# Kernel optimization log

Hardware: AMD Instinct MI355X
Metric: run time of the kernel (lower is better)

Reference implementation:

```python
import jax, jax.numpy as jnp
import numpy as np

B, S, D, H, DFF = 2, 2048, 768, 12, 3072
HD = D // H
LN_EPS = 1e-5


def _layernorm(x, g, b):
    mu = jnp.mean(x, axis=-1, keepdims=True)
    var = jnp.mean((x - mu) ** 2, axis=-1, keepdims=True)
    return (x - mu) * jax.lax.rsqrt(var + LN_EPS) * g + b


def setup_inputs() -> dict:
    key = jax.random.key(0)
    ks = jax.random.split(key, 16)
    s_d = 1.0 / np.sqrt(D)
    s_ff = 1.0 / np.sqrt(DFF)
    return {
        "x": jax.random.normal(ks[0], (B, S, D), jnp.float32),
        "alibi_bias": jax.random.normal(ks[1], (H, S, S), jnp.float32) * 0.1,
        "Wq": jax.random.normal(ks[2], (D, D), jnp.float32) * s_d,
        "bq": jnp.zeros((D,), jnp.float32),
        "Wk": jax.random.normal(ks[3], (D, D), jnp.float32) * s_d,
        "bk": jnp.zeros((D,), jnp.float32),
        "Wv": jax.random.normal(ks[4], (D, D), jnp.float32) * s_d,
        "bv": jnp.zeros((D,), jnp.float32),
        "Wo": jax.random.normal(ks[5], (D, D), jnp.float32) * s_d,
        "bo": jnp.zeros((D,), jnp.float32),
        "W1": jax.random.normal(ks[6], (D, DFF), jnp.float32) * s_d,
        "b1": jnp.zeros((DFF,), jnp.float32),
        "W2": jax.random.normal(ks[7], (DFF, D), jnp.float32) * s_ff,
        "b2": jnp.zeros((D,), jnp.float32),
        "g1": jnp.ones((D,), jnp.float32),
        "be1": jnp.zeros((D,), jnp.float32),
        "g2": jnp.ones((D,), jnp.float32),
        "be2": jnp.zeros((D,), jnp.float32),
    }


def reference(x, alibi_bias, Wq, bq, Wk, bk, Wv, bv, Wo, bo, W1, b1, W2, b2, g1, be1, g2, be2):
    # QKV projections -> (B, H, S, HD)
    def split_heads(t):
        return t.reshape(B, S, H, HD).transpose(0, 2, 1, 3)

    q = split_heads(x @ Wq + bq)
    k = split_heads(x @ Wk + bk)
    v = split_heads(x @ Wv + bv)

    # causal mask (S, S): -inf above diagonal
    causal = jnp.where(jnp.triu(jnp.ones((S, S), bool), k=1), -jnp.inf, 0.0).astype(x.dtype)
    mask = alibi_bias[None] + causal[None, None]  # (1, H, S, S) broadcast over batch

    scale = 1.0 / np.sqrt(HD)
    scores = jnp.einsum("bhqd,bhkd->bhqk", q, k) * scale + mask
    probs = jax.nn.softmax(scores, axis=-1)
    attn = jnp.einsum("bhqk,bhkd->bhqd", probs, v)  # (B, H, S, HD)
    attn = attn.transpose(0, 2, 1, 3).reshape(B, S, D)
    attn = attn @ Wo + bo

    x = _layernorm(x + attn, g1, be1)
    ff = jax.nn.relu(x @ W1 + b1) @ W2 + b2
    x = _layernorm(x + ff, g2, be2)
    return x
```

## Files before the change

kernel.cpp:

```cpp
#include <hip/hip_runtime.h>
#include <hip/hip_bf16.h>

#define BB 2
#define SS 2048
#define DD 768
#define HH 12
#define HD 64
#define DFF 3072
#define NROW (BB * SS)
#define QLD  2304
#define LN_EPS 1e-5f
#define NSPLIT 4

typedef __attribute__((ext_vector_type(8))) short bf16x8;
typedef __attribute__((ext_vector_type(4))) short bf16x4;
typedef __attribute__((ext_vector_type(4))) float f32x4;

__device__ __forceinline__ void gll16(const void* g, void* l) {
    __builtin_amdgcn_global_load_lds(
        (const __attribute__((address_space(1))) unsigned int*)g,
        (__attribute__((address_space(3))) unsigned int*)l,
        16, 0, 0);
}

__device__ __forceinline__ unsigned short bf16bits(float f) {
    __hip_bfloat16 h = __float2bfloat16(f);
    return *(unsigned short*)&h;
}

__device__ __forceinline__ float bf16tof(unsigned short u) {
    unsigned int ui = ((unsigned int)u) << 16;
    return __uint_as_float(ui);
}

__device__ __forceinline__ float block_sum(float v, float* red) {
    __syncthreads();
    #pragma unroll
    for (int off = 32; off > 0; off >>= 1) v += __shfl_down(v, off, 64);
    if ((threadIdx.x & 63) == 0) red[threadIdx.x >> 6] = v;
    __syncthreads();
    if (threadIdx.x == 0) red[0] = red[0] + red[1] + red[2] + red[3];
    __syncthreads();
    return red[0];
}

template<int TM, int TN>
__global__ __launch_bounds__(256) void mfma_gemm(
        const __hip_bfloat16* __restrict__ A, const __hip_bfloat16* __restrict__ BT,
        const float* __restrict__ bias, float* __restrict__ Cf,
        __hip_bfloat16* __restrict__ Cb,
        int N, int K, int relu, int bf16out, int qscale_cols) {
    constexpr int BK = 64;
    constexpr int MW = TM / 32;
    constexpr int NW = TN / 32;
    __shared__ __hip_bfloat16 a_s[TM * BK];
    __shared__ __hip_bfloat16 b_s[TN * BK];

    const int tid  = threadIdx.x;
    const int lane = tid & 63;
    const int wid  = tid >> 6;
    const int wm   = (wid & 1) * (TM / 2);
    const int wn   = (wid >> 1) * (TN / 2);
    const int qq   = lane & 15;
    const int quad = lane >> 4;

    const int nwg  = (int)(gridDim.x * gridDim.y);
    const int dlin = (int)blockIdx.x + (int)gridDim.x * (int)blockIdx.y;
    const int wsw  = (dlin & 7) * (nwg >> 3) + (dlin >> 3);
    const int m0 = (wsw / (int)gridDim.x) * TM;
    const int n0 = (wsw % (int)gridDim.x) * TN;

    const int r8   = lane >> 3;
    const int u8   = lane & 7;
    const int gcol = ((u8 ^ r8) << 3);

    f32x4 acc[MW][NW] = {};

    for (int k0 = 0; k0 < K; k0 += BK) {
        const __hip_bfloat16* Ag = A + (size_t)m0 * K + k0 + gcol;
        #pragma unroll
        for (int i = 0; i < TM / 32; i++) {
            const int row = i * 32 + wid * 8 + r8;
            gll16(Ag + (size_t)row * K, a_s + row * BK + u8 * 8);
        }
        const __hip_bfloat16* Bg = BT + (size_t)n0 * K + k0 + gcol;
        #pragma unroll
        for (int i = 0; i < TN / 32; i++) {
            const int row = i * 32 + wid * 8 + r8;
            gll16(Bg + (size_t)row * K, b_s + row * BK + u8 * 8);
        }
        __syncthreads();

        #pragma unroll
        for (int kh = 0; kh < 2; kh++) {
            const int ku = kh * 4 + quad;
            bf16x8 af[MW], bfr[NW];
            #pragma unroll
            for (int mi = 0; mi < MW; mi++) {
                const int row = wm + mi * 16 + qq;
                af[mi] = *(const bf16x8*)(a_s + row * BK + ((ku ^ (qq & 7)) << 3));
            }
            #pragma unroll
            for (int ni = 0; ni < NW; ni++) {
                const int row = wn + ni * 16 + qq;
                bfr[ni] = *(const bf16x8*)(b_s + row * BK + ((ku ^ (qq & 7)) << 3));
            }
            #pragma unroll
            for (int mi = 0; mi < MW; mi++)
                #pragma unroll
                for (int ni = 0; ni < NW; ni++)
                    acc[mi][ni] = __builtin_amdgcn_mfma_f32_16x16x32_bf16(
                            af[mi], bfr[ni], acc[mi][ni], 0, 0, 0);
        }
        __syncthreads();
    }

    #pragma unroll
    for (int mi = 0; mi < MW; mi++) {
        #pragma unroll
        for (int ni = 0; ni < NW; ni++) {
            const int col = n0 + wn + ni * 16 + qq;
            const float bv = bias[col];
            const float sc = (col < qscale_cols) ? 0.125f : 1.0f;
            #pragma unroll
            for (int r = 0; r < 4; r++) {
                const int row = m0 + wm + mi * 16 + quad * 4 + r;
                float v = acc[mi][ni][r] + bv;
                if (relu) v = fmaxf(v, 0.f);
                v *= sc;
                if (bf16out) Cb[(size_t)row * N + col] = __float2bfloat16(v);
                else         Cf[(size_t)row * N + col] = v;
            }
        }
    }
}

__device__ __forceinline__ void transpose_tile(
        const float* __restrict__ in, __hip_bfloat16* __restrict__ out,
        int K, int N, int tix, int tiy, float (*t)[33]) {
    const int n0 = tix * 32;
    const int k0 = tiy * 32;
    const int r = threadIdx.x >> 3;
    const int c = threadIdx.x & 7;
    float4 v = *(const float4*)&in[(size_t)(k0 + r) * N + n0 + c * 4];
    t[r][c * 4 + 0] = v.x;
    t[r][c * 4 + 1] = v.y;
    t[r][c * 4 + 2] = v.z;
    t[r][c * 4 + 3] = v.w;
    __syncthreads();
    union { unsigned short u[4]; uint2 w; } pk;
    #pragma unroll
    for (int j = 0; j < 4; j++) pk.u[j] = bf16bits(t[c * 4 + j][r]);
    *(uint2*)&out[(size_t)(n0 + r) * K + k0 + c * 4] = pk.w;
}

__global__ __launch_bounds__(256) void prep_kernel(
        const float* __restrict__ Wq, const float* __restrict__ Wk,
        const float* __restrict__ Wv, const float* __restrict__ Wo,
        const float* __restrict__ W1, const float* __restrict__ W2,
        const float* __restrict__ bq, const float* __restrict__ bk,
        const float* __restrict__ bv, const float* __restrict__ x,
        __hip_bfloat16* __restrict__ WqkvT, __hip_bfloat16* __restrict__ WoT,
        __hip_bfloat16* __restrict__ W1T, __hip_bfloat16* __restrict__ W2T,
        float* __restrict__ biasc, __hip_bfloat16* __restrict__ xb) {
    __shared__ float t[32][33];
    const int bx = blockIdx.x;
    if (bx < 2304) {
        const int wsel = bx / 576;
        const int r = bx - wsel * 576;
        const float* in = (wsel == 0) ? Wq : (wsel == 1) ? Wk : (wsel == 2) ? Wv : Wo;
        __hip_bfloat16* out = (wsel == 3) ? WoT : WqkvT + (size_t)wsel * DD * DD;
        transpose_tile(in, out, DD, DD, r % 24, r / 24, t);
    } else if (bx < 4608) {
        const int r = bx - 2304;
        transpose_tile(W1, W1T, DD, DFF, r % 96, r / 96, t);
    } else if (bx < 6912) {
        const int r = bx - 4608;
        transpose_tile(W2, W2T, DFF, DD, r % 24, r / 24, t);
    } else if (bx < 9984) {
        const int i = (bx - 6912) * 256 + threadIdx.x;
        float4 v = ((const float4*)x)[i];
        union { unsigned short u[4]; uint2 w; } pk;
        pk.u[0] = bf16bits(v.x); pk.u[1] = bf16bits(v.y);
        pk.u[2] = bf16bits(v.z); pk.u[3] = bf16bits(v.w);
        ((uint2*)xb)[i] = pk.w;
    } else {
        const int i = (bx - 9984) * 256 + threadIdx.x;
        if (i < QLD)
            biasc[i] = (i < DD) ? bq[i] : ((i < 2 * DD) ? bk[i - DD] : bv[i - 2 * DD]);
    }
}

__global__ __launch_bounds__(256) void flash_attn_kernel(
        const __hip_bfloat16* __restrict__ QKV, const float* __restrict__ alibi,
        __hip_bfloat16* __restrict__ Opart, float* __restrict__ ml) {
    const int gx   = (int)gridDim.x;
    const int nwg  = gx * (int)(gridDim.y * gridDim.z);
    const int dlin = (int)blockIdx.x +
                     gx * ((int)blockIdx.y + (int)gridDim.y * (int)blockIdx.z);
    const int wsw  = (dlin & 7) * (nwg >> 3) + (dlin >> 3);
    const int rb   = wsw % gx;
    const int hb   = wsw / gx;
    const int h    = hb % HH;
    const int b    = hb / HH;
    const int qt   = gx / NSPLIT - 1 - rb / NSPLIT;
    const int s    = rb & (NSPLIT - 1);

    const int tid  = threadIdx.x;
    const int lane = tid & 63;
    const int w    = tid >> 6;
    const int qq   = lane & 15;
    const int quad = lane >> 4;
    const int q0   = qt * 64;

    __shared__ unsigned short K_s[64 * 72];
    __shared__ unsigned short V_t[64 * 72];
    __shared__ unsigned short P_t[4][16 * 72];

    const size_t qrow = ((size_t)(b * SS + q0 + w * 16 + qq)) * QLD + (size_t)h * HD;
    const bf16x8 qf0 = *(const bf16x8*)(QKV + qrow + quad * 8);
    const bf16x8 qf1 = *(const bf16x8*)(QKV + qrow + 32 + quad * 8);

    f32x4 O[4] = {};
    float m_i = -1e30f, l_i = 0.f;

    const float* alrow = alibi + ((size_t)h * SS + q0 + w * 16 + qq) * SS;
    const size_t kvrow0 = (size_t)(b * SS) * QLD + (size_t)h * HD + w * 16;
    const int lim = q0 + w * 16 + qq;

    for (int t = s; t * 64 <= q0; t += NSPLIT) {
        const int k0 = t * 64;
        __syncthreads();

        {
            const size_t kv = kvrow0 + (size_t)(k0 + lane) * QLD;
            bf16x8 kv0 = *(const bf16x8*)(QKV + DD + kv);
            bf16x8 kv1 = *(const bf16x8*)(QKV + DD + kv + 8);
            *(bf16x8*)&K_s[lane * 72 + w * 16]     = kv0;
            *(bf16x8*)&K_s[lane * 72 + w * 16 + 8] = kv1;
            bf16x8 vv0 = *(const bf16x8*)(QKV + 2 * DD + kv);
            bf16x8 vv1 = *(const bf16x8*)(QKV + 2 * DD + kv + 8);
            #pragma unroll
            for (int j = 0; j < 8; j++) {
                V_t[(w * 16 + j) * 72 + lane]     = vv0[j];
                V_t[(w * 16 + 8 + j) * 72 + lane] = vv1[j];
            }
        }
        __syncthreads();

        float4 av[4];
        #pragma unroll
        for (int c = 0; c < 4; c++)
            av[c] = *(const float4*)(alrow + k0 + c * 16 + quad * 4);

        __builtin_amdgcn_s_setprio(1);
        f32x4 S[4];
        #pragma unroll
        for (int c = 0; c < 4; c++) {
            f32x4 sacc = {};
            bf16x8 kf0 = *(const bf16x8*)&K_s[(c * 16 + qq) * 72 + quad * 8];
            bf16x8 kf1 = *(const bf16x8*)&K_s[(c * 16 + qq) * 72 + 32 + quad * 8];
            sacc = __builtin_amdgcn_mfma_f32_16x16x32_bf16(kf0, qf0, sacc, 0, 0, 0);
            sacc = __builtin_amdgcn_mfma_f32_16x16x32_bf16(kf1, qf1, sacc, 0, 0, 0);
            S[c] = sacc;
        }
        __builtin_amdgcn_s_setprio(0);

        float sv[16];
        float smax = -1e30f;
        const int klim = lim - k0;
        #pragma unroll
        for (int c = 0; c < 4; c++) {
            #pragma unroll
            for (int r = 0; r < 4; r++) {
                const int key = c * 16 + quad * 4 + r;
                float sc = S[c][r] + ((const float*)&av[c])[r];
                if (key > klim) sc = -1e30f;
                sv[c * 4 + r] = sc;
                smax = fmaxf(smax, sc);
            }
        }
        smax = fmaxf(smax, __shfl_xor(smax, 16));
        smax = fmaxf(smax, __shfl_xor(smax, 32));

        const float nm = fmaxf(m_i, smax);
        const float alpha = __expf(m_i - nm);
        float lsum = 0.f;
        #pragma unroll
        for (int i = 0; i < 16; i++) {
            const float e = __expf(sv[i] - nm);
            sv[i] = e;
            lsum += e;
        }
        lsum += __shfl_xor(lsum, 16);
        lsum += __shfl_xor(lsum, 32);
        l_i = l_i * alpha + lsum;
        m_i = nm;

        #pragma unroll
        for (int c = 0; c < 4; c++) {
            bf16x4 pk;
            #pragma unroll
            for (int r = 0; r < 4; r++) pk[r] = (short)bf16bits(sv[c * 4 + r]);
            *(bf16x4*)&P_t[w][qq * 72 + c * 16 + quad * 4] = pk;
        }

        #pragma unroll
        for (int r = 0; r < 4; r++) {
            const float ar = __shfl(alpha, quad * 4 + r);
            #pragma unroll
            for (int d = 0; d < 4; d++) O[d][r] *= ar;
        }

        const bf16x8 pf0 = *(const bf16x8*)&P_t[w][qq * 72 + quad * 8];
        const bf16x8 pf1 = *(const bf16x8*)&P_t[w][qq * 72 + 32 + quad * 8];
        __builtin_amdgcn_s_setprio(1);
        #pragma unroll
        for (int d0 = 0; d0 < 4; d0++) {
            bf16x8 vf0 = *(const bf16x8*)&V_t[(d0 * 16 + qq) * 72 + quad * 8];
            bf16x8 vf1 = *(const bf16x8*)&V_t[(d0 * 16 + qq) * 72 + 32 + quad * 8];
            O[d0] = __builtin_amdgcn_mfma_f32_16x16x32_bf16(pf0, vf0, O[d0], 0, 0, 0);
            O[d0] = __builtin_amdgcn_mfma_f32_16x16x32_bf16(pf1, vf1, O[d0], 0, 0, 0);
        }
        __builtin_amdgcn_s_setprio(0);
    }

    if (quad == 0) {
        float* mlp = ml + (((size_t)(b * SS + q0 + w * 16 + qq) * HH + h) * NSPLIT + s) * 2;
        mlp[0] = m_i;
        mlp[1] = l_i;
    }
    #pragma unroll
    for (int r = 0; r < 4; r++) {
        const int row = q0 + w * 16 + quad * 4 + r;
        __hip_bfloat16* op = Opart +
            (((size_t)(b * SS + row) * HH + h) * NSPLIT + s) * 64 + qq;
        op[0]  = __float2bfloat16(O[0][r]);
        op[16] = __float2bfloat16(O[1][r]);
        op[32] = __float2bfloat16(O[2][r]);
        op[48] = __float2bfloat16(O[3][r]);
    }
}

__global__ __launch_bounds__(256) void attn_combine_kernel(
        const __hip_bfloat16* __restrict__ Opart, const float* __restrict__ ml,
        __hip_bfloat16* __restrict__ attnb) {
    const int idx = blockIdx.x * 256 + threadIdx.x;
    const int rr  = idx / 96;
    const int rem = idx - rr * 96;
    const int h   = rem >> 3;
    const int d8  = (rem & 7) * 8;
    const size_t base = ((size_t)rr * HH + h) * NSPLIT;
    float ms[NSPLIT], ls[NSPLIT];
    float m = -1e30f;
    #pragma unroll
    for (int s = 0; s < NSPLIT; s++) {
        ms[s] = ml[(base + s) * 2];
        ls[s] = ml[(base + s) * 2 + 1];
        m = fmaxf(m, ms[s]);
    }
    float es[NSPLIT], denom = 0.f;
    #pragma unroll
    for (int s = 0; s < NSPLIT; s++) {
        es[s] = __expf(ms[s] - m);
        denom += ls[s] * es[s];
    }
    const float inv = 1.f / denom;
    float acc[8] = {};
    #pragma unroll
    for (int s = 0; s < NSPLIT; s++) {
        const bf16x8 o = *(const bf16x8*)(Opart + (base + s) * 64 + d8);
        #pragma unroll
        for (int j = 0; j < 8; j++)
            acc[j] += bf16tof((unsigned short)o[j]) * es[s];
    }
    union { unsigned short u[8]; bf16x8 v; } pk;
    #pragma unroll
    for (int j = 0; j < 8; j++) pk.u[j] = bf16bits(acc[j] * inv);
    *(bf16x8*)(attnb + (size_t)rr * DD + h * 64 + d8) = pk.v;
}

__global__ __launch_bounds__(256) void ln_kernel(
        const float* __restrict__ a, const float* __restrict__ r,
        const float* __restrict__ g, const float* __restrict__ beta,
        float* __restrict__ outf, __hip_bfloat16* __restrict__ outb) {
    const int row = blockIdx.x;
    const int tid = threadIdx.x;
    __shared__ float red[64];

    float vals[3];
    float s = 0.f;
    #pragma unroll
    for (int i = 0; i < 3; i++) {
        const int col = i * 256 + tid;
        float t = a[(size_t)row * DD + col] + r[(size_t)row * DD + col];
        vals[i] = t;
        s += t;
    }
    const float mean = block_sum(s, red) * (1.f / DD);

    float s2 = 0.f;
    #pragma unroll
    for (int i = 0; i < 3; i++) {
        float d = vals[i] - mean;
        s2 += d * d;
    }
    const float var = block_sum(s2, red) * (1.f / DD);
    const float rstd = rsqrtf(var + LN_EPS);

    #pragma unroll
    for (int i = 0; i < 3; i++) {
        const int col = i * 256 + tid;
        const float o = (vals[i] - mean) * rstd * g[col] + beta[col];
        outf[(size_t)row * DD + col] = o;
        if (outb) outb[(size_t)row * DD + col] = __float2bfloat16(o);
    }
}

extern "C" void kernel_launch(void* const* d_in, const int* in_sizes, int n_in,
                              void* d_out, int out_size, void* d_ws, size_t ws_size,
                              hipStream_t stream) {
    const float* x     = (const float*)d_in[0];
    const float* alibi = (const float*)d_in[1];
    const float* Wq = (const float*)d_in[2];
    const float* bq = (const float*)d_in[3];
    const float* Wk = (const float*)d_in[4];
    const float* bk = (const float*)d_in[5];
    const float* Wv = (const float*)d_in[6];
    const float* bv = (const float*)d_in[7];
    const float* Wo = (const float*)d_in[8];
    const float* bo = (const float*)d_in[9];
    const float* W1 = (const float*)d_in[10];
    const float* b1 = (const float*)d_in[11];
    const float* W2 = (const float*)d_in[12];
    const float* b2 = (const float*)d_in[13];
    const float* g1 = (const float*)d_in[14];
    const float* be1 = (const float*)d_in[15];
    const float* g2 = (const float*)d_in[16];
    const float* be2 = (const float*)d_in[17];
    float* out = (float*)d_out;

    char* p = (char*)d_ws;
    auto alloc = [&](size_t bytes) { char* r = p; p += (bytes + 255) & ~(size_t)255; return r; };
    __hip_bfloat16* WqkvT = (__hip_bfloat16*)alloc((size_t)QLD * DD * 2);
    __hip_bfloat16* WoT   = (__hip_bfloat16*)alloc((size_t)DD * DD * 2);
    __hip_bfloat16* W1T   = (__hip_bfloat16*)alloc((size_t)DFF * DD * 2);
    __hip_bfloat16* W2T   = (__hip_bfloat16*)alloc((size_t)DD * DFF * 2);
    float*          biasc = (float*)alloc((size_t)QLD * 4);
    __hip_bfloat16* xb    = (__hip_bfloat16*)alloc((size_t)NROW * DD * 2);
    __hip_bfloat16* qkvb  = (__hip_bfloat16*)alloc((size_t)NROW * DFF * 2);
    __hip_bfloat16* attnb = (__hip_bfloat16*)alloc((size_t)NROW * DD * 2);
    float*          proj  = (float*)alloc((size_t)NROW * DD * 4);
    float*          ln1   = (float*)alloc((size_t)NROW * DD * 4);
    __hip_bfloat16* ln1b  = xb;
    __hip_bfloat16* ff1b  = qkvb;
    float*          ff2   = proj;

    __hip_bfloat16* Opart = (__hip_bfloat16*)proj;
    float*          mlbuf = (float*)xb;

    const dim3 blk(256);

    prep_kernel<<<dim3(9993), blk, 0, stream>>>(
            Wq, Wk, Wv, Wo, W1, W2, bq, bk, bv, x,
            WqkvT, WoT, W1T, W2T, biasc, xb);

    mfma_gemm<128, 96><<<dim3(QLD / 96, NROW / 128), blk, 0, stream>>>(
            xb, WqkvT, biasc, nullptr, qkvb, QLD, DD, 0, 1, DD);

    flash_attn_kernel<<<dim3(NSPLIT * (SS / 64), HH, BB), blk, 0, stream>>>(
            qkvb, alibi, Opart, mlbuf);
    attn_combine_kernel<<<dim3(NROW * 96 / 256), blk, 0, stream>>>(
            Opart, mlbuf, attnb);

    mfma_gemm<64, 64><<<dim3(DD / 64, NROW / 64), blk, 0, stream>>>(
            attnb, WoT, bo, proj, nullptr, DD, DD, 0, 0, 0);

    ln_kernel<<<dim3(NROW), blk, 0, stream>>>(x, proj, g1, be1, ln1, ln1b);

    mfma_gemm<128, 128><<<dim3(DFF / 128, NROW / 128), blk, 0, stream>>>(
            ln1b, W1T, b1, nullptr, ff1b, DFF, DD, 1, 1, 0);
    mfma_gemm<64, 64><<<dim3(DD / 64, NROW / 64), blk, 0, stream>>>(
            ff1b, W2T, b2, ff2, nullptr, DD, DFF, 0, 0, 0);

    ln_kernel<<<dim3(NROW), blk, 0, stream>>>(ln1, ff2, g2, be2, out, nullptr);
}
```

Baseline: 478.8 us.

## Add 256x256-tile 512-thread GEMM with XCD swizzle for QKV and FF1

Adds a new bf16 MFMA GEMM kernel with 256x256 output tiles, 8 waves per block, double-buffered LDS fed by global_load_lds with an XOR swizzle, and a block-index remap that spreads consecutive tiles across XCDs. It replaces the 128x96 QKV projection and the 128x128 FF1 GEMM. Larger tiles raise arithmetic intensity and cut redundant global loads. The cost is far fewer blocks: QKV gets 9x16=144 and FF1 12x16=192, against a 256-CU device. It also needs 128KB of LDS per block and heavy accumulator register use, which may limit occupancy.

```diff
diff --git a/kernel.cpp b/kernel.cpp
--- a/kernel.cpp
+++ b/kernel.cpp
@@ -130,6 +130,99 @@
                 v *= sc;
                 if (bf16out) Cb[(size_t)row * N + col] = __float2bfloat16(v);
                 else         Cf[(size_t)row * N + col] = v;
+            }
+        }
+    }
+}
+
+__global__ __launch_bounds__(512) void mfma_gemm_256(
+        const __hip_bfloat16* __restrict__ A, const __hip_bfloat16* __restrict__ BT,
+        const float* __restrict__ bias, __hip_bfloat16* __restrict__ Cb,
+        int N, int K, int relu, int qscale_cols) {
+    constexpr int BK = 64;
+    __shared__ __hip_bfloat16 a_s[2][256 * BK];
+    __shared__ __hip_bfloat16 b_s[2][256 * BK];
+
+    const int tid  = threadIdx.x;
+    const int lane = tid & 63;
+    const int wid  = tid >> 6;
+    const int wm   = (wid >> 2) * 128;
+    const int wn   = (wid & 3) * 64;
+    const int qq   = lane & 15;
+    const int quad = lane >> 4;
+
+    const int gx   = (int)gridDim.x;
+    const int nwg  = gx * (int)gridDim.y;
+    const int dlin = (int)blockIdx.x + gx * (int)blockIdx.y;
+    const int wsw  = (dlin & 7) * (nwg >> 3) + (dlin >> 3);
+    const int m0 = (wsw / gx) * 256;
+    const int n0 = (wsw % gx) * 256;
+
+    const int srow = tid >> 3;
+    const int u8   = tid & 7;
+    const int gcol = ((u8 ^ (srow & 7)) << 3);
+
+    auto stage = [&](int buf, int k0) {
+        const __hip_bfloat16* Ag = A + (size_t)m0 * K + k0 + gcol;
+        #pragma unroll
+        for (int i = 0; i < 4; i++) {
+            const int row = i * 64 + srow;
+            gll16(Ag + (size_t)row * K, &a_s[buf][row * BK + u8 * 8]);
+        }
+        const __hip_bfloat16* Bg = BT + (size_t)n0 * K + k0 + gcol;
+        #pragma unroll
+        for (int i = 0; i < 4; i++) {
+            const int row = i * 64 + srow;
+            gll16(Bg + (size_t)row * K, &b_s[buf][row * BK + u8 * 8]);
+        }
+    };
+
+    f32x4 acc[8][4] = {};
+    const int NT = K / BK;
+
+    stage(0, 0);
+    __syncthreads();
+    int cur = 0;
+    for (int t = 0; t < NT; t++) {
+        if (t + 1 < NT) stage(cur ^ 1, (t + 1) * BK);
+        const __hip_bfloat16* as = a_s[cur];
+        const __hip_bfloat16* bs = b_s[cur];
+        #pragma unroll
+        for (int kh = 0; kh < 2; kh++) {
+            const int ko = ((kh * 4 + quad) ^ (qq & 7)) << 3;
+            bf16x8 af[8], bfr[4];
+            #pragma unroll
+            for (int mi = 0; mi < 8; mi++)
+                af[mi] = *(const bf16x8*)(as + (wm + mi * 16 + qq) * BK + ko);
+            #pragma unroll
+            for (int ni = 0; ni < 4; ni++)
+                bfr[ni] = *(const bf16x8*)(bs + (wn + ni * 16 + qq) * BK + ko);
+            __builtin_amdgcn_s_setprio(1);
+            #pragma unroll
+            for (int mi = 0; mi < 8; mi++)
+                #pragma unroll
+                for (int ni = 0; ni < 4; ni++)
+                    acc[mi][ni] = __builtin_amdgcn_mfma_f32_16x16x32_bf16(
+                            af[mi], bfr[ni], acc[mi][ni], 0, 0, 0);
+            __builtin_amdgcn_s_setprio(0);
+        }
+        __syncthreads();
+        cur ^= 1;
+    }
+
+    #pragma unroll
+    for (int mi = 0; mi < 8; mi++) {
+        #pragma unroll
+        for (int ni = 0; ni < 4; ni++) {
+            const int col = n0 + wn + ni * 16 + qq;
+            const float bv = bias[col];
+            const float sc = (col < qscale_cols) ? 0.125f : 1.0f;
+            #pragma unroll
+            for (int r = 0; r < 4; r++) {
+                const int row = m0 + wm + mi * 16 + quad * 4 + r;
+                float v = acc[mi][ni][r] + bv;
+                if (relu) v = fmaxf(v, 0.f);
+                Cb[(size_t)row * N + col] = __float2bfloat16(v * sc);
             }
         }
     }
@@ -460,13 +553,14 @@
     float*          mlbuf = (float*)xb;
 
     const dim3 blk(256);
+    const dim3 blk512(512);
 
     prep_kernel<<<dim3(9993), blk, 0, stream>>>(
             Wq, Wk, Wv, Wo, W1, W2, bq, bk, bv, x,
             WqkvT, WoT, W1T, W2T, biasc, xb);
 
-    mfma_gemm<128, 96><<<dim3(QLD / 96, NROW / 128), blk, 0, stream>>>(
-            xb, WqkvT, biasc, nullptr, qkvb, QLD, DD, 0, 1, DD);
+    mfma_gemm_256<<<dim3(QLD / 256, NROW / 256), blk512, 0, stream>>>(
+            xb, WqkvT, biasc, qkvb, QLD, DD, 0, DD);
 
     flash_attn_kernel<<<dim3(NSPLIT * (SS / 64), HH, BB), blk, 0, stream>>>(
             qkvb, alibi, Opart, mlbuf);
@@ -478,8 +572,8 @@
 
     ln_kernel<<<dim3(NROW), blk, 0, stream>>>(x, proj, g1, be1, ln1, ln1b);
 
-    mfma_gemm<128, 128><<<dim3(DFF / 128, NROW / 128), blk, 0, stream>>>(
-            ln1b, W1T, b1, nullptr, ff1b, DFF, DD, 1, 1, 0);
+    mfma_gemm_256<<<dim3(DFF / 256, NROW / 256), blk512, 0, stream>>>(
+            ln1b, W1T, b1, ff1b, DFF, DD, 1, 0);
     mfma_gemm<64, 64><<<dim3(DD / 64, NROW / 64), blk, 0, stream>>>(
             ff1b, W2T, b2, ff2, nullptr, DD, DFF, 0, 0, 0);
 
```

After: 484.3 us. Within noise of the previous version (+1.2%).
